# Optimization experiments

Hardware: AMD Instinct MI355X
Metric: run time of the kernel (lower is better)

## Reference

```python
import jax, jax.numpy as jnp
import numpy as np

E = 1024   # embed_dim
H = 16     # num_heads
HD = E // H
FF = 4096  # hidden_dim
EPS = 1e-5

def _ln(x, g, b):
    mu = jnp.mean(x, axis=-1, keepdims=True)
    var = jnp.mean((x - mu) ** 2, axis=-1, keepdims=True)
    return (x - mu) * jax.lax.rsqrt(var + EPS) * g + b

def setup_inputs() -> dict:
    key = jax.random.key(0)
    ks = jax.random.split(key, 8)
    s = 0.02
    return {
        "x": jax.random.normal(ks[0], (2, 2048, E), dtype=jnp.float32),
        "w_qkv": jax.random.normal(ks[1], (3 * E, E), dtype=jnp.float32) * s,
        "b_qkv": jnp.zeros((3 * E,), dtype=jnp.float32),
        "w_out": jax.random.normal(ks[2], (E, E), dtype=jnp.float32) * s,
        "b_out": jnp.zeros((E,), dtype=jnp.float32),
        "g1": jnp.ones((E,), dtype=jnp.float32),
        "beta1": jnp.zeros((E,), dtype=jnp.float32),
        "g2": jnp.ones((E,), dtype=jnp.float32),
        "beta2": jnp.zeros((E,), dtype=jnp.float32),
        "w1": jax.random.normal(ks[3], (FF, E), dtype=jnp.float32) * s,
        "bf1": jnp.zeros((FF,), dtype=jnp.float32),
        "w2": jax.random.normal(ks[4], (E, FF), dtype=jnp.float32) * s,
        "bf2": jnp.zeros((E,), dtype=jnp.float32),
    }

def reference(x, w_qkv, b_qkv, w_out, b_out, g1, beta1, g2, beta2, w1, bf1, w2, bf2):
    B, S, _ = x.shape
    # qkv projection, then the module's exact reshape: (B,S,H,3*HD) -> (H,B,S,3*HD)
    qkv = (x @ w_qkv.T + b_qkv).reshape(B, S, H, 3 * HD).transpose(2, 0, 1, 3)
    q, k, v = jnp.split(qkv, 3, axis=-1)           # each (H,B,S,HD)
    scores = jnp.einsum('hbqd,hbkd->hbqk', q, k) / (HD ** 0.5)
    attn = jax.nn.softmax(scores, axis=-1)
    ctx = jnp.einsum('hbqk,hbkd->hbqd', attn, v)   # (H,B,S,HD)
    ctx = ctx.transpose(1, 2, 0, 3).reshape(B, S, E)
    attn_out = ctx @ w_out.T + b_out
    x1 = _ln(x + attn_out, g1, beta1)
    # FFN with exact (erf-based) GELU, matching torch nn.GELU default
    h = jax.nn.gelu(x1 @ w1.T + bf1, approximate=False)
    ffn_out = h @ w2.T + bf2
    return _ln(x1 + ffn_out, g2, beta2)
```

## Files before the change

### kernel.cpp

```cpp
#include <hip/hip_runtime.h>
#include <hip/hip_bf16.h>
#include <math.h>

typedef __bf16 bf16x8 __attribute__((ext_vector_type(8)));
typedef __bf16 bf16x4 __attribute__((ext_vector_type(4)));
typedef float  f32x4  __attribute__((ext_vector_type(4)));

#define MFMA16(a, b, c) __builtin_amdgcn_mfma_f32_16x16x32_bf16((a), (b), (c), 0, 0, 0)

__device__ __forceinline__ void gl16(const void* g, void* l) {
  __builtin_amdgcn_global_load_lds(
      (const __attribute__((address_space(1))) unsigned int*)g,
      (__attribute__((address_space(3))) unsigned int*)l, 16, 0, 0);
}

__global__ __launch_bounds__(256) void cast_all(
    const float* __restrict__ x, const float* __restrict__ wqkv,
    const float* __restrict__ wout, const float* __restrict__ w1,
    const float* __restrict__ w2, __bf16* __restrict__ xb,
    __bf16* __restrict__ wqkvb, __bf16* __restrict__ woutb,
    __bf16* __restrict__ w1b, __bf16* __restrict__ w2b) {
  const long i = ((long)blockIdx.x * 256 + threadIdx.x) * 4;
  const float* src;
  __bf16* dst;
  long off;
  if (i < 4194304L) { src = x; dst = xb; off = i; }
  else if (i < 7340032L) { src = wqkv; dst = wqkvb; off = i - 4194304L; }
  else if (i < 8388608L) { src = wout; dst = woutb; off = i - 7340032L; }
  else if (i < 12582912L) { src = w1; dst = w1b; off = i - 8388608L; }
  else { src = w2; dst = w2b; off = i - 12582912L; }
  const float4 f = *(const float4*)(src + off);
  bf16x4 o = {(__bf16)f.x, (__bf16)f.y, (__bf16)f.z, (__bf16)f.w};
  *(bf16x4*)(dst + off) = o;
}

template <int MODE>
__global__ __launch_bounds__(256, 2) void gemm_bt(
    const __bf16* __restrict__ A, const __bf16* __restrict__ Bw,
    const float* __restrict__ bias, __bf16* __restrict__ outB,
    int M, int N, int K) {
  __shared__ __bf16 AsL[128 * 32], AsH[128 * 32];
  __shared__ __bf16 BsL[128 * 32], BsH[128 * 32];
  const int tid = threadIdx.x;
  const int wave = tid >> 6, lane = tid & 63;
  const int quad = lane >> 4, l16 = lane & 15;
  const int wm = (wave >> 1) * 64, wn = (wave & 1) * 64;
  const long bm = (long)blockIdx.y * 128, bn = (long)blockIdx.x * 128;
  const int r0 = tid >> 2;
  const int c0 = (tid & 3) * 8;
  const __bf16* Ag = A + (bm + r0) * (long)K + c0;
  const __bf16* Bg = Bw + (bn + r0) * (long)K + c0;

  f32x4 acc[4][4] = {};

  for (int k0 = 0; k0 < K; k0 += 64) {
    __syncthreads();
    gl16(Ag + k0, &AsL[tid * 8]);
    gl16(Ag + 64 * (long)K + k0, &AsL[2048 + tid * 8]);
    gl16(Ag + k0 + 32, &AsH[tid * 8]);
    gl16(Ag + 64 * (long)K + k0 + 32, &AsH[2048 + tid * 8]);
    gl16(Bg + k0, &BsL[tid * 8]);
    gl16(Bg + 64 * (long)K + k0, &BsL[2048 + tid * 8]);
    gl16(Bg + k0 + 32, &BsH[tid * 8]);
    gl16(Bg + 64 * (long)K + k0 + 32, &BsH[2048 + tid * 8]);
    __syncthreads();

    bf16x8 afL[4], afH[4], bfL[4], bfH[4];
#pragma unroll
    for (int mt = 0; mt < 4; mt++) {
      afL[mt] = *(const bf16x8*)&AsL[(wm + mt * 16 + l16) * 32 + quad * 8];
      afH[mt] = *(const bf16x8*)&AsH[(wm + mt * 16 + l16) * 32 + quad * 8];
    }
#pragma unroll
    for (int nt = 0; nt < 4; nt++) {
      bfL[nt] = *(const bf16x8*)&BsL[(wn + nt * 16 + l16) * 32 + quad * 8];
      bfH[nt] = *(const bf16x8*)&BsH[(wn + nt * 16 + l16) * 32 + quad * 8];
    }
#pragma unroll
    for (int nt = 0; nt < 4; nt++)
#pragma unroll
      for (int mt = 0; mt < 4; mt++) {
        acc[mt][nt] = MFMA16(afL[mt], bfL[nt], acc[mt][nt]);
        acc[mt][nt] = MFMA16(afH[mt], bfH[nt], acc[mt][nt]);
      }
  }

#pragma unroll
  for (int mt = 0; mt < 4; mt++) {
#pragma unroll
    for (int nt = 0; nt < 4; nt++) {
#pragma unroll
      for (int r = 0; r < 4; r++) {
        const int row = (int)bm + wm + mt * 16 + quad * 4 + r;
        const int col = (int)bn + wn + nt * 16 + l16;
        float v = acc[mt][nt][r] + bias[col];
        if (MODE == 0) {
          const int b = row >> 11, s = row & 2047;
          const int h = col / 192, rem = col - h * 192;
          const int seg = rem >> 6, d = rem & 63;
          const int hb = h * 2 + b;
          if (seg == 0) {
            v *= 0.180336880111113704f;
            outB[((long)hb * 2048 + s) * 64 + d] = (__bf16)v;
          } else if (seg == 1) {
            outB[4194304L + ((long)hb * 2048 + s) * 64 + d] = (__bf16)v;
          } else {
            const int t = s >> 6, kp = s & 63;
            outB[2 * 4194304L + (((long)hb * 32 + t) * 64 + d) * 64 + kp] = (__bf16)v;
          }
        } else {
          const float g = 0.5f * v * (1.0f + erff(v * 0.70710678118654752f));
          outB[(long)row * N + col] = (__bf16)g;
        }
      }
    }
  }
}

__global__ __launch_bounds__(256, 2) void gemm_split(
    const __bf16* __restrict__ A, const __bf16* __restrict__ Bw,
    __bf16* __restrict__ Pbase, const long4 offs, int N, int K, int splitK) {
  __shared__ __bf16 AsL[128 * 32], AsH[128 * 32];
  __shared__ __bf16 BsL[128 * 32], BsH[128 * 32];
  const int tid = threadIdx.x;
  const int wave = tid >> 6, lane = tid & 63;
  const int quad = lane >> 4, l16 = lane & 15;
  const int wm = (wave >> 1) * 64, wn = (wave & 1) * 64;
  const long bm = (long)blockIdx.y * 128, bn = (long)blockIdx.x * 128;
  const int z = blockIdx.z;
  const long kb = (long)z * splitK;
  const int r0 = tid >> 2;
  const int c0 = (tid & 3) * 8;
  const __bf16* Ag = A + (bm + r0) * (long)K + c0 + kb;
  const __bf16* Bg = Bw + (bn + r0) * (long)K + c0 + kb;

  f32x4 acc[4][4] = {};

  for (int k0 = 0; k0 < splitK; k0 += 64) {
    __syncthreads();
    gl16(Ag + k0, &AsL[tid * 8]);
    gl16(Ag + 64 * (long)K + k0, &AsL[2048 + tid * 8]);
    gl16(Ag + k0 + 32, &AsH[tid * 8]);
    gl16(Ag + 64 * (long)K + k0 + 32, &AsH[2048 + tid * 8]);
    gl16(Bg + k0, &BsL[tid * 8]);
    gl16(Bg + 64 * (long)K + k0, &BsL[2048 + tid * 8]);
    gl16(Bg + k0 + 32, &BsH[tid * 8]);
    gl16(Bg + 64 * (long)K + k0 + 32, &BsH[2048 + tid * 8]);
    __syncthreads();

    bf16x8 afL[4], afH[4], bfL[4], bfH[4];
#pragma unroll
    for (int mt = 0; mt < 4; mt++) {
      afL[mt] = *(const bf16x8*)&AsL[(wm + mt * 16 + l16) * 32 + quad * 8];
      afH[mt] = *(const bf16x8*)&AsH[(wm + mt * 16 + l16) * 32 + quad * 8];
    }
#pragma unroll
    for (int nt = 0; nt < 4; nt++) {
      bfL[nt] = *(const bf16x8*)&BsL[(wn + nt * 16 + l16) * 32 + quad * 8];
      bfH[nt] = *(const bf16x8*)&BsH[(wn + nt * 16 + l16) * 32 + quad * 8];
    }
#pragma unroll
    for (int nt = 0; nt < 4; nt++)
#pragma unroll
      for (int mt = 0; mt < 4; mt++) {
        acc[mt][nt] = MFMA16(afL[mt], bfL[nt], acc[mt][nt]);
        acc[mt][nt] = MFMA16(afH[mt], bfH[nt], acc[mt][nt]);
      }
  }

  const long po = (z == 0) ? offs.x : (z == 1) ? offs.y : (z == 2) ? offs.z : offs.w;
#pragma unroll
  for (int mt = 0; mt < 4; mt++)
#pragma unroll
    for (int nt = 0; nt < 4; nt++)
#pragma unroll
      for (int r = 0; r < 4; r++) {
        const int row = (int)bm + wm + mt * 16 + quad * 4 + r;
        const int col = (int)bn + wn + nt * 16 + l16;
        Pbase[po + (long)row * N + col] = (__bf16)acc[mt][nt][r];
      }
}

template <int WB>
__global__ __launch_bounds__(256) void reduce_ln(
    const __bf16* __restrict__ Pbase, const long4 offs,
    const float* __restrict__ resid, const float* __restrict__ bias,
    const float* __restrict__ g, const float* __restrict__ be,
    float* __restrict__ outF, __bf16* __restrict__ outB) {
  const int tid = threadIdx.x;
  const long row = blockIdx.x;
  const int c = tid * 4;
  float4 v = ((const float4*)(resid + row * 1024))[tid];
  const float4 bb = ((const float4*)bias)[tid];
  v.x += bb.x; v.y += bb.y; v.z += bb.z; v.w += bb.w;
  const long lo[4] = {offs.x, offs.y, offs.z, offs.w};
#pragma unroll
  for (int s = 0; s < 4; s++) {
    const bf16x4 p = *(const bf16x4*)&Pbase[lo[s] + row * 1024 + c];
    v.x += (float)p[0]; v.y += (float)p[1]; v.z += (float)p[2]; v.w += (float)p[3];
  }
  float sum = v.x + v.y + v.z + v.w;
  float sq = v.x * v.x + v.y * v.y + v.z * v.z + v.w * v.w;
#pragma unroll
  for (int m = 32; m >= 1; m >>= 1) {
    sum += __shfl_xor(sum, m);
    sq += __shfl_xor(sq, m);
  }
  __shared__ float red[8];
  const int wave = tid >> 6;
  if ((tid & 63) == 0) {
    red[wave] = sum;
    red[4 + wave] = sq;
  }
  __syncthreads();
  sum = red[0] + red[1] + red[2] + red[3];
  sq = red[4] + red[5] + red[6] + red[7];
  const float mu = sum * (1.f / 1024.f);
  const float var = sq * (1.f / 1024.f) - mu * mu;
  const float rs = rsqrtf(var + 1e-5f);
  const float4 gv = ((const float4*)g)[tid];
  const float4 bv = ((const float4*)be)[tid];
  float4 o;
  o.x = (v.x - mu) * rs * gv.x + bv.x;
  o.y = (v.y - mu) * rs * gv.y + bv.y;
  o.z = (v.z - mu) * rs * gv.z + bv.z;
  o.w = (v.w - mu) * rs * gv.w + bv.w;
  ((float4*)(outF + row * 1024))[tid] = o;
  if (WB) {
    bf16x4 ob = {(__bf16)o.x, (__bf16)o.y, (__bf16)o.z, (__bf16)o.w};
    *(bf16x4*)&outB[row * 1024 + c] = ob;
  }
}

__global__ __launch_bounds__(256) void flash_attn(const __bf16* __restrict__ Qb,
                                                  const __bf16* __restrict__ Kb,
                                                  const __bf16* __restrict__ Vtb,
                                                  __bf16* __restrict__ ctx) {
  __shared__ __bf16 KsLo[64 * 32], KsHi[64 * 32];
  __shared__ __bf16 VsLo[64 * 32], VsHi[64 * 32];
  __shared__ __bf16 Pb[4][32 * 68];
  const int tid = threadIdx.x;
  const int wave = tid >> 6, lane = tid & 63;
  const int quad = lane >> 4, l16 = lane & 15;
  const int n = blockIdx.x;
  const int hb = n & 31;
  const int qblk = n >> 5;
  const int h = hb >> 1, b = hb & 1;
  const __bf16* Q = Qb + (long)hb * 131072;
  const __bf16* K = Kb + (long)hb * 131072;
  const __bf16* Vt = Vtb + (long)hb * 131072;
  const int qr = qblk * 128 + wave * 32;

  bf16x8 q0[2], q1[2];
#pragma unroll
  for (int rb = 0; rb < 2; rb++) {
    q0[rb] = *(const bf16x8*)&Q[(qr + rb * 16 + l16) * 64 + quad * 8];
    q1[rb] = *(const bf16x8*)&Q[(qr + rb * 16 + l16) * 64 + 32 + quad * 8];
  }

  f32x4 o[2][4] = {};
  f32x4 lp[2] = {};

  const int sr = tid >> 2;
  const int sc = (tid & 3) * 8;

  for (int kt = 0; kt < 2048; kt += 64) {
    __syncthreads();
    gl16(&K[(kt + sr) * 64 + sc], &KsLo[tid * 8]);
    gl16(&K[(kt + sr) * 64 + 32 + sc], &KsHi[tid * 8]);
    const __bf16* Vtile = Vt + (long)(kt >> 6) * 4096;
    gl16(&Vtile[sr * 64 + sc], &VsLo[tid * 8]);
    gl16(&Vtile[sr * 64 + 32 + sc], &VsHi[tid * 8]);
    __syncthreads();

    bf16x8 kf0[4], kf1[4];
#pragma unroll
    for (int nt = 0; nt < 4; nt++) {
      kf0[nt] = *(const bf16x8*)&KsLo[(nt * 16 + l16) * 32 + quad * 8];
      kf1[nt] = *(const bf16x8*)&KsHi[(nt * 16 + l16) * 32 + quad * 8];
    }
    f32x4 s[2][4];
#pragma unroll
    for (int rb = 0; rb < 2; rb++)
#pragma unroll
      for (int nt = 0; nt < 4; nt++) {
        f32x4 z = {};
        z = MFMA16(q0[rb], kf0[nt], z);
        z = MFMA16(q1[rb], kf1[nt], z);
        s[rb][nt] = z;
      }

#pragma unroll
    for (int rb = 0; rb < 2; rb++)
#pragma unroll
      for (int nt = 0; nt < 4; nt++)
#pragma unroll
        for (int r = 0; r < 4; r++) {
          const float p = __builtin_amdgcn_exp2f(s[rb][nt][r]);
          s[rb][nt][r] = p;
          lp[rb][r] += p;
        }

#pragma unroll
    for (int rb = 0; rb < 2; rb++)
#pragma unroll
      for (int nt = 0; nt < 4; nt++)
#pragma unroll
        for (int r = 0; r < 4; r++)
          Pb[wave][(rb * 16 + quad * 4 + r) * 68 + nt * 16 + l16] =
              (__bf16)s[rb][nt][r];

    bf16x8 vf0[4], vf1[4];
#pragma unroll
    for (int nt = 0; nt < 4; nt++) {
      vf0[nt] = *(const bf16x8*)&VsLo[(nt * 16 + l16) * 32 + quad * 8];
      vf1[nt] = *(const bf16x8*)&VsHi[(nt * 16 + l16) * 32 + quad * 8];
    }
#pragma unroll
    for (int rb = 0; rb < 2; rb++) {
      const int pbase = (rb * 16 + l16) * 68;
      const bf16x4 pa0 = *(const bf16x4*)&Pb[wave][pbase + quad * 8];
      const bf16x4 pa1 = *(const bf16x4*)&Pb[wave][pbase + quad * 8 + 4];
      const bf16x4 pb0 = *(const bf16x4*)&Pb[wave][pbase + 32 + quad * 8];
      const bf16x4 pb1 = *(const bf16x4*)&Pb[wave][pbase + 32 + quad * 8 + 4];
      const bf16x8 p0 = __builtin_shufflevector(pa0, pa1, 0, 1, 2, 3, 4, 5, 6, 7);
      const bf16x8 p1 = __builtin_shufflevector(pb0, pb1, 0, 1, 2, 3, 4, 5, 6, 7);
#pragma unroll
      for (int nt = 0; nt < 4; nt++) {
        o[rb][nt] = MFMA16(p0, vf0[nt], o[rb][nt]);
        o[rb][nt] = MFMA16(p1, vf1[nt], o[rb][nt]);
      }
    }
  }

#pragma unroll
  for (int rb = 0; rb < 2; rb++) {
    float inv[4];
#pragma unroll
    for (int r = 0; r < 4; r++) {
      float l = lp[rb][r];
      l += __shfl_xor(l, 1);
      l += __shfl_xor(l, 2);
      l += __shfl_xor(l, 4);
      l += __shfl_xor(l, 8);
      inv[r] = __builtin_amdgcn_rcpf(l);
    }
#pragma unroll
    for (int nt = 0; nt < 4; nt++)
#pragma unroll
      for (int r = 0; r < 4; r++) {
        const int srow = qr + rb * 16 + quad * 4 + r;
        const float val = o[rb][nt][r] * inv[r];
        const int d = nt * 16 + l16;
        ctx[((long)(b * 2048 + srow)) * 1024 + h * 64 + d] = (__bf16)val;
      }
  }
}

extern "C" void kernel_launch(void* const* d_in, const int* in_sizes, int n_in,
                              void* d_out, int out_size, void* d_ws, size_t ws_size,
                              hipStream_t stream) {
  const float* x     = (const float*)d_in[0];
  const float* w_qkv = (const float*)d_in[1];
  const float* b_qkv = (const float*)d_in[2];
  const float* w_out = (const float*)d_in[3];
  const float* b_out = (const float*)d_in[4];
  const float* g1    = (const float*)d_in[5];
  const float* be1   = (const float*)d_in[6];
  const float* g2    = (const float*)d_in[7];
  const float* be2   = (const float*)d_in[8];
  const float* w1    = (const float*)d_in[9];
  const float* bf1   = (const float*)d_in[10];
  const float* w2    = (const float*)d_in[11];
  const float* bf2   = (const float*)d_in[12];
  float* out = (float*)d_out;

  char* ws = (char*)d_ws;
  const long MB = 1024L * 1024;
  __bf16* wsb   = (__bf16*)ws;
  __bf16* wqkvb = (__bf16*)(ws + 0 * MB);
  __bf16* woutb = (__bf16*)(ws + 6 * MB);
  __bf16* w1b   = (__bf16*)(ws + 8 * MB);
  __bf16* w2b   = (__bf16*)(ws + 16 * MB);
  __bf16* xb    = (__bf16*)(ws + 24 * MB);
  __bf16* qkvb  = (__bf16*)(ws + 32 * MB);
  __bf16* ctxb  = (__bf16*)(ws + 56 * MB);
  float*  res1  = (float*)(ws + 64 * MB);
  __bf16* x1b   = (__bf16*)(ws + 80 * MB);
  __bf16* hb    = (__bf16*)(ws + 24 * MB);

  const long4 offs_op = {24 * 524288L, 32 * 524288L, 40 * 524288L, 48 * 524288L};
  const long4 offs_f2 = {0 * 524288L, 8 * 524288L, 56 * 524288L, 80 * 524288L};

  cast_all<<<16384, 256, 0, stream>>>(x, w_qkv, w_out, w1, w2,
                                      xb, wqkvb, woutb, w1b, w2b);

  gemm_bt<0><<<dim3(24, 32), 256, 0, stream>>>(xb, wqkvb, b_qkv, qkvb,
                                               4096, 3072, 1024);
  flash_attn<<<512, 256, 0, stream>>>(qkvb, qkvb + 4194304,
                                      qkvb + 2 * 4194304, ctxb);
  gemm_split<<<dim3(8, 32, 4), 256, 0, stream>>>(ctxb, woutb, wsb, offs_op,
                                                 1024, 1024, 256);
  reduce_ln<1><<<4096, 256, 0, stream>>>(wsb, offs_op, x, b_out, g1, be1,
                                         res1, x1b);
  gemm_bt<2><<<dim3(32, 32), 256, 0, stream>>>(x1b, w1b, bf1, hb,
                                               4096, 4096, 1024);
  gemm_split<<<dim3(8, 32, 4), 256, 0, stream>>>(hb, w2b, wsb, offs_f2,
                                                 1024, 4096, 1024);
  reduce_ln<0><<<4096, 256, 0, stream>>>(wsb, offs_f2, res1, bf2, g2, be2,
                                         out, nullptr);
}
```

Measured before the change: 357.1 us.

## Split flash attention over key halves and add a combine kernel

Each attention block now processes only half of the key sequence, doubling the grid so more compute units are busy. Unnormalized partial outputs (bf16) and row sums are written to workspace, and a new combine kernel sums the two halves, normalizes, and writes ctx in the original layout. This works without max tracking because the softmax has no max subtraction. It costs an extra launch, extra memory traffic for the partials, and slightly more rounding.

```diff
diff --git a/kernel.cpp b/kernel.cpp
--- a/kernel.cpp
+++ b/kernel.cpp
@@ -235,7 +235,8 @@
 __global__ __launch_bounds__(256) void flash_attn(const __bf16* __restrict__ Qb,
                                                   const __bf16* __restrict__ Kb,
                                                   const __bf16* __restrict__ Vtb,
-                                                  __bf16* __restrict__ ctx) {
+                                                  __bf16* __restrict__ Opart,
+                                                  float* __restrict__ Lpart) {
   __shared__ __bf16 KsLo[64 * 32], KsHi[64 * 32];
   __shared__ __bf16 VsLo[64 * 32], VsHi[64 * 32];
   __shared__ __bf16 Pb[4][32 * 68];
@@ -244,8 +245,8 @@
   const int quad = lane >> 4, l16 = lane & 15;
   const int n = blockIdx.x;
   const int hb = n & 31;
-  const int qblk = n >> 5;
-  const int h = hb >> 1, b = hb & 1;
+  const int z = (n >> 5) & 1;
+  const int qblk = n >> 6;
   const __bf16* Q = Qb + (long)hb * 131072;
   const __bf16* K = Kb + (long)hb * 131072;
   const __bf16* Vt = Vtb + (long)hb * 131072;
@@ -264,7 +265,8 @@
   const int sr = tid >> 2;
   const int sc = (tid & 3) * 8;
 
-  for (int kt = 0; kt < 2048; kt += 64) {
+  const int kend = z * 1024 + 1024;
+  for (int kt = z * 1024; kt < kend; kt += 64) {
     __syncthreads();
     gl16(&K[(kt + sr) * 64 + sc], &KsLo[tid * 8]);
     gl16(&K[(kt + sr) * 64 + 32 + sc], &KsHi[tid * 8]);
@@ -284,10 +286,10 @@
     for (int rb = 0; rb < 2; rb++)
 #pragma unroll
       for (int nt = 0; nt < 4; nt++) {
-        f32x4 z = {};
-        z = MFMA16(q0[rb], kf0[nt], z);
-        z = MFMA16(q1[rb], kf1[nt], z);
-        s[rb][nt] = z;
+        f32x4 zz = {};
+        zz = MFMA16(q0[rb], kf0[nt], zz);
+        zz = MFMA16(q1[rb], kf1[nt], zz);
+        s[rb][nt] = zz;
       }
 
 #pragma unroll
@@ -333,9 +335,10 @@
     }
   }
 
+  const long zb = (long)z * 4194304;
 #pragma unroll
   for (int rb = 0; rb < 2; rb++) {
-    float inv[4];
+    float lred[4];
 #pragma unroll
     for (int r = 0; r < 4; r++) {
       float l = lp[rb][r];
@@ -343,18 +346,42 @@
       l += __shfl_xor(l, 2);
       l += __shfl_xor(l, 4);
       l += __shfl_xor(l, 8);
-      inv[r] = __builtin_amdgcn_rcpf(l);
-    }
-#pragma unroll
-    for (int nt = 0; nt < 4; nt++)
+      lred[r] = l;
+    }
+    if (l16 == 0) {
 #pragma unroll
       for (int r = 0; r < 4; r++) {
         const int srow = qr + rb * 16 + quad * 4 + r;
-        const float val = o[rb][nt][r] * inv[r];
+        Lpart[z * 65536 + hb * 2048 + srow] = lred[r];
+      }
+    }
+#pragma unroll
+    for (int nt = 0; nt < 4; nt++)
+#pragma unroll
+      for (int r = 0; r < 4; r++) {
+        const int srow = qr + rb * 16 + quad * 4 + r;
         const int d = nt * 16 + l16;
-        ctx[((long)(b * 2048 + srow)) * 1024 + h * 64 + d] = (__bf16)val;
-      }
-  }
+        Opart[zb + ((long)hb * 2048 + srow) * 64 + d] = (__bf16)o[rb][nt][r];
+      }
+  }
+}
+
+__global__ __launch_bounds__(256) void flash_combine(
+    const __bf16* __restrict__ Opart, const float* __restrict__ Lpart,
+    __bf16* __restrict__ ctx) {
+  const int g = blockIdx.x * 256 + threadIdx.x;
+  const int hbrow = g >> 3;
+  const int d0 = (g & 7) * 8;
+  const int hb = hbrow >> 11, srow = hbrow & 2047;
+  const int h = hb >> 1, b = hb & 1;
+  const bf16x8 o1 = *(const bf16x8*)&Opart[(long)hbrow * 64 + d0];
+  const bf16x8 o2 = *(const bf16x8*)&Opart[4194304L + (long)hbrow * 64 + d0];
+  const float inv = __builtin_amdgcn_rcpf(Lpart[hbrow] + Lpart[65536 + hbrow]);
+  bf16x8 r;
+#pragma unroll
+  for (int j = 0; j < 8; j++)
+    r[j] = (__bf16)(((float)o1[j] + (float)o2[j]) * inv);
+  *(bf16x8*)&ctx[((long)(b * 2048 + srow)) * 1024 + h * 64 + d0] = r;
 }
 
 extern "C" void kernel_launch(void* const* d_in, const int* in_sizes, int n_in,
@@ -388,6 +415,8 @@
   float*  res1  = (float*)(ws + 64 * MB);
   __bf16* x1b   = (__bf16*)(ws + 80 * MB);
   __bf16* hb    = (__bf16*)(ws + 24 * MB);
+  __bf16* opart = (__bf16*)(ws + 64 * MB);
+  float*  lpart = (float*)(ws + 80 * MB);
 
   const long4 offs_op = {24 * 524288L, 32 * 524288L, 40 * 524288L, 48 * 524288L};
   const long4 offs_f2 = {0 * 524288L, 8 * 524288L, 56 * 524288L, 80 * 524288L};
@@ -397,8 +426,9 @@
 
   gemm_bt<0><<<dim3(24, 32), 256, 0, stream>>>(xb, wqkvb, b_qkv, qkvb,
                                                4096, 3072, 1024);
-  flash_attn<<<512, 256, 0, stream>>>(qkvb, qkvb + 4194304,
-                                      qkvb + 2 * 4194304, ctxb);
+  flash_attn<<<1024, 256, 0, stream>>>(qkvb, qkvb + 4194304,
+                                       qkvb + 2 * 4194304, opart, lpart);
+  flash_combine<<<2048, 256, 0, stream>>>(opart, lpart, ctxb);
   gemm_split<<<dim3(8, 32, 4), 256, 0, stream>>>(ctxb, woutb, wsb, offs_op,
                                                  1024, 1024, 256);
   reduce_ln<1><<<4096, 256, 0, stream>>>(wsb, offs_op, x, b_out, g1, be1,
```

Result: slower. 371.0 us (+3.9%).

## Double-buffer LDS tiles in GEMM and flash-attention loops to overlap loads

Applied to the files above, without the earlier changes.

The shared-memory tiles in gemm_bt, gemm_split and flash_attn now have two buffers each. The loads for the next K or KV tile are issued right after the loop-top barrier, while the current tile is being computed. This removes one barrier per iteration and is meant to hide global-to-LDS latency behind the MFMA work. In exchange the GEMM kernels use twice the LDS (64KB per block), which may limit how many blocks fit on a compute unit.

```diff
diff --git a/kernel.cpp b/kernel.cpp
--- a/kernel.cpp
+++ b/kernel.cpp
@@ -34,13 +34,23 @@
   *(bf16x4*)(dst + off) = o;
 }
 
+#define STAGE_GEMM(buf, kk)                                          \
+  gl16(Ag + (kk), &AsL[buf][tid * 8]);                               \
+  gl16(Ag + 64 * (long)K + (kk), &AsL[buf][2048 + tid * 8]);         \
+  gl16(Ag + (kk) + 32, &AsH[buf][tid * 8]);                          \
+  gl16(Ag + 64 * (long)K + (kk) + 32, &AsH[buf][2048 + tid * 8]);    \
+  gl16(Bg + (kk), &BsL[buf][tid * 8]);                               \
+  gl16(Bg + 64 * (long)K + (kk), &BsL[buf][2048 + tid * 8]);         \
+  gl16(Bg + (kk) + 32, &BsH[buf][tid * 8]);                          \
+  gl16(Bg + 64 * (long)K + (kk) + 32, &BsH[buf][2048 + tid * 8]);
+
 template <int MODE>
 __global__ __launch_bounds__(256, 2) void gemm_bt(
     const __bf16* __restrict__ A, const __bf16* __restrict__ Bw,
     const float* __restrict__ bias, __bf16* __restrict__ outB,
     int M, int N, int K) {
-  __shared__ __bf16 AsL[128 * 32], AsH[128 * 32];
-  __shared__ __bf16 BsL[128 * 32], BsH[128 * 32];
+  __shared__ __bf16 AsL[2][4096], AsH[2][4096];
+  __shared__ __bf16 BsL[2][4096], BsH[2][4096];
   const int tid = threadIdx.x;
   const int wave = tid >> 6, lane = tid & 63;
   const int quad = lane >> 4, l16 = lane & 15;
@@ -53,28 +63,22 @@
 
   f32x4 acc[4][4] = {};
 
-  for (int k0 = 0; k0 < K; k0 += 64) {
+  STAGE_GEMM(0, 0);
+  int ib = 0;
+  for (int k0 = 0; k0 < K; k0 += 64, ib ^= 1) {
     __syncthreads();
-    gl16(Ag + k0, &AsL[tid * 8]);
-    gl16(Ag + 64 * (long)K + k0, &AsL[2048 + tid * 8]);
-    gl16(Ag + k0 + 32, &AsH[tid * 8]);
-    gl16(Ag + 64 * (long)K + k0 + 32, &AsH[2048 + tid * 8]);
-    gl16(Bg + k0, &BsL[tid * 8]);
-    gl16(Bg + 64 * (long)K + k0, &BsL[2048 + tid * 8]);
-    gl16(Bg + k0 + 32, &BsH[tid * 8]);
-    gl16(Bg + 64 * (long)K + k0 + 32, &BsH[2048 + tid * 8]);
-    __syncthreads();
+    if (k0 + 64 < K) { STAGE_GEMM(ib ^ 1, k0 + 64); }
 
     bf16x8 afL[4], afH[4], bfL[4], bfH[4];
 #pragma unroll
     for (int mt = 0; mt < 4; mt++) {
-      afL[mt] = *(const bf16x8*)&AsL[(wm + mt * 16 + l16) * 32 + quad * 8];
-      afH[mt] = *(const bf16x8*)&AsH[(wm + mt * 16 + l16) * 32 + quad * 8];
+      afL[mt] = *(const bf16x8*)&AsL[ib][(wm + mt * 16 + l16) * 32 + quad * 8];
+      afH[mt] = *(const bf16x8*)&AsH[ib][(wm + mt * 16 + l16) * 32 + quad * 8];
     }
 #pragma unroll
     for (int nt = 0; nt < 4; nt++) {
-      bfL[nt] = *(const bf16x8*)&BsL[(wn + nt * 16 + l16) * 32 + quad * 8];
-      bfH[nt] = *(const bf16x8*)&BsH[(wn + nt * 16 + l16) * 32 + quad * 8];
+      bfL[nt] = *(const bf16x8*)&BsL[ib][(wn + nt * 16 + l16) * 32 + quad * 8];
+      bfH[nt] = *(const bf16x8*)&BsH[ib][(wn + nt * 16 + l16) * 32 + quad * 8];
     }
 #pragma unroll
     for (int nt = 0; nt < 4; nt++)
@@ -120,8 +124,8 @@
 __global__ __launch_bounds__(256, 2) void gemm_split(
     const __bf16* __restrict__ A, const __bf16* __restrict__ Bw,
     __bf16* __restrict__ Pbase, const long4 offs, int N, int K, int splitK) {
-  __shared__ __bf16 AsL[128 * 32], AsH[128 * 32];
-  __shared__ __bf16 BsL[128 * 32], BsH[128 * 32];
+  __shared__ __bf16 AsL[2][4096], AsH[2][4096];
+  __shared__ __bf16 BsL[2][4096], BsH[2][4096];
   const int tid = threadIdx.x;
   const int wave = tid >> 6, lane = tid & 63;
   const int quad = lane >> 4, l16 = lane & 15;
@@ -136,28 +140,22 @@
 
   f32x4 acc[4][4] = {};
 
-  for (int k0 = 0; k0 < splitK; k0 += 64) {
+  STAGE_GEMM(0, 0);
+  int ib = 0;
+  for (int k0 = 0; k0 < splitK; k0 += 64, ib ^= 1) {
     __syncthreads();
-    gl16(Ag + k0, &AsL[tid * 8]);
-    gl16(Ag + 64 * (long)K + k0, &AsL[2048 + tid * 8]);
-    gl16(Ag + k0 + 32, &AsH[tid * 8]);
-    gl16(Ag + 64 * (long)K + k0 + 32, &AsH[2048 + tid * 8]);
-    gl16(Bg + k0, &BsL[tid * 8]);
-    gl16(Bg + 64 * (long)K + k0, &BsL[2048 + tid * 8]);
-    gl16(Bg + k0 + 32, &BsH[tid * 8]);
-    gl16(Bg + 64 * (long)K + k0 + 32, &BsH[2048 + tid * 8]);
-    __syncthreads();
+    if (k0 + 64 < splitK) { STAGE_GEMM(ib ^ 1, k0 + 64); }
 
     bf16x8 afL[4], afH[4], bfL[4], bfH[4];
 #pragma unroll
     for (int mt = 0; mt < 4; mt++) {
-      afL[mt] = *(const bf16x8*)&AsL[(wm + mt * 16 + l16) * 32 + quad * 8];
-      afH[mt] = *(const bf16x8*)&AsH[(wm + mt * 16 + l16) * 32 + quad * 8];
+      afL[mt] = *(const bf16x8*)&AsL[ib][(wm + mt * 16 + l16) * 32 + quad * 8];
+      afH[mt] = *(const bf16x8*)&AsH[ib][(wm + mt * 16 + l16) * 32 + quad * 8];
     }
 #pragma unroll
     for (int nt = 0; nt < 4; nt++) {
-      bfL[nt] = *(const bf16x8*)&BsL[(wn + nt * 16 + l16) * 32 + quad * 8];
-      bfH[nt] = *(const bf16x8*)&BsH[(wn + nt * 16 + l16) * 32 + quad * 8];
+      bfL[nt] = *(const bf16x8*)&BsL[ib][(wn + nt * 16 + l16) * 32 + quad * 8];
+      bfH[nt] = *(const bf16x8*)&BsH[ib][(wn + nt * 16 + l16) * 32 + quad * 8];
     }
 #pragma unroll
     for (int nt = 0; nt < 4; nt++)
@@ -232,12 +230,21 @@
   }
 }
 
+#define STAGE_FA(buf, kk)                                            \
+  gl16(&K[((kk) + sr) * 64 + sc], &KsLo[buf][tid * 8]);              \
+  gl16(&K[((kk) + sr) * 64 + 32 + sc], &KsHi[buf][tid * 8]);         \
+  {                                                                  \
+    const __bf16* Vtile = Vt + (long)((kk) >> 6) * 4096;             \
+    gl16(&Vtile[sr * 64 + sc], &VsLo[buf][tid * 8]);                 \
+    gl16(&Vtile[sr * 64 + 32 + sc], &VsHi[buf][tid * 8]);            \
+  }
+
 __global__ __launch_bounds__(256) void flash_attn(const __bf16* __restrict__ Qb,
                                                   const __bf16* __restrict__ Kb,
                                                   const __bf16* __restrict__ Vtb,
                                                   __bf16* __restrict__ ctx) {
-  __shared__ __bf16 KsLo[64 * 32], KsHi[64 * 32];
-  __shared__ __bf16 VsLo[64 * 32], VsHi[64 * 32];
+  __shared__ __bf16 KsLo[2][2048], KsHi[2][2048];
+  __shared__ __bf16 VsLo[2][2048], VsHi[2][2048];
   __shared__ __bf16 Pb[4][32 * 68];
   const int tid = threadIdx.x;
   const int wave = tid >> 6, lane = tid & 63;
@@ -264,30 +271,27 @@
   const int sr = tid >> 2;
   const int sc = (tid & 3) * 8;
 
-  for (int kt = 0; kt < 2048; kt += 64) {
+  STAGE_FA(0, 0);
+  int ib = 0;
+  for (int kt = 0; kt < 2048; kt += 64, ib ^= 1) {
     __syncthreads();
-    gl16(&K[(kt + sr) * 64 + sc], &KsLo[tid * 8]);
-    gl16(&K[(kt + sr) * 64 + 32 + sc], &KsHi[tid * 8]);
-    const __bf16* Vtile = Vt + (long)(kt >> 6) * 4096;
-    gl16(&Vtile[sr * 64 + sc], &VsLo[tid * 8]);
-    gl16(&Vtile[sr * 64 + 32 + sc], &VsHi[tid * 8]);
-    __syncthreads();
+    if (kt + 64 < 2048) { STAGE_FA(ib ^ 1, kt + 64); }
 
     bf16x8 kf0[4], kf1[4];
 #pragma unroll
     for (int nt = 0; nt < 4; nt++) {
-      kf0[nt] = *(const bf16x8*)&KsLo[(nt * 16 + l16) * 32 + quad * 8];
-      kf1[nt] = *(const bf16x8*)&KsHi[(nt * 16 + l16) * 32 + quad * 8];
+      kf0[nt] = *(const bf16x8*)&KsLo[ib][(nt * 16 + l16) * 32 + quad * 8];
+      kf1[nt] = *(const bf16x8*)&KsHi[ib][(nt * 16 + l16) * 32 + quad * 8];
     }
     f32x4 s[2][4];
 #pragma unroll
     for (int rb = 0; rb < 2; rb++)
 #pragma unroll
       for (int nt = 0; nt < 4; nt++) {
-        f32x4 z = {};
-        z = MFMA16(q0[rb], kf0[nt], z);
-        z = MFMA16(q1[rb], kf1[nt], z);
-        s[rb][nt] = z;
+        f32x4 zz = {};
+        zz = MFMA16(q0[rb], kf0[nt], zz);
+        zz = MFMA16(q1[rb], kf1[nt], zz);
+        s[rb][nt] = zz;
       }
 
 #pragma unroll
@@ -313,8 +317,8 @@
     bf16x8 vf0[4], vf1[4];
 #pragma unroll
     for (int nt = 0; nt < 4; nt++) {
-      vf0[nt] = *(const bf16x8*)&VsLo[(nt * 16 + l16) * 32 + quad * 8];
-      vf1[nt] = *(const bf16x8*)&VsHi[(nt * 16 + l16) * 32 + quad * 8];
+      vf0[nt] = *(const bf16x8*)&VsLo[ib][(nt * 16 + l16) * 32 + quad * 8];
+      vf1[nt] = *(const bf16x8*)&VsHi[ib][(nt * 16 + l16) * 32 + quad * 8];
     }
 #pragma unroll
     for (int rb = 0; rb < 2; rb++) {
```

Measured after the change: 386.1 us. 8.1% more time.
